# Kernel tuning notes

Measured on AMD Instinct MI355X. Metric: run time of the kernel, lower is better.

The kernel has to match this reference:

```python
import jax, jax.numpy as jnp
import numpy as np

B, S, T, E, H = 64, 128, 128, 512, 1024


def setup_inputs() -> dict:
    key = jax.random.key(0)
    ks = jax.random.split(key, 12)

    def lin(k, shape, fan_in):
        return jax.random.normal(k, shape, jnp.float32) / np.float32(np.sqrt(fan_in))

    return {
        "trg_embed": jax.random.normal(ks[0], (B, T, E), jnp.float32),
        "encoder_hidden": jax.random.normal(ks[1], (B, S, 2 * H), jnp.float32),
        "encoder_final": jax.random.normal(ks[2], (B, 2 * H), jnp.float32),
        "src_mask": jnp.ones((B, S), dtype=bool),
        # BahdanauAttention params (all bias=False)
        "key_W": lin(ks[3], (H, 2 * H), 2 * H),      # proj_key = enc_hidden @ key_W.T
        "query_W": lin(ks[4], (H, H), H),
        "energy_w": lin(ks[5], (H,), H),             # energy_layer Linear(H, 1)
        # GRU (single layer) params, PyTorch layout [3H, in] with gate order r,z,n
        "W_ih": lin(ks[6], (3 * H, E + 2 * H), E + 2 * H),
        "W_hh": lin(ks[7], (3 * H, H), H),
        "b_ih": jnp.zeros((3 * H,), jnp.float32),
        "b_hh": jnp.zeros((3 * H,), jnp.float32),
        # bridge Linear(2H, H, bias=True)
        "bridge_W": lin(ks[8], (H, 2 * H), 2 * H),
        "bridge_b": jnp.zeros((H,), jnp.float32),
        # pre_output_layer Linear(H + 2H + E, H, bias=False)
        "preout_W": lin(ks[9], (H, 3 * H + E), 3 * H + E),
    }


def reference(trg_embed, encoder_hidden, encoder_final, src_mask,
              key_W, query_W, energy_w, W_ih, W_hh, b_ih, b_hh,
              bridge_W, bridge_b, preout_W):
    # Precompute attention keys once: [B, S, H]
    proj_key = jnp.einsum('bsd,hd->bsh', encoder_hidden, key_W)
    # init_hidden: tanh(bridge(encoder_final)) -> [B, H]
    h0 = jnp.tanh(encoder_final @ bridge_W.T + bridge_b)
    neg = jnp.asarray(-1e9, trg_embed.dtype)

    def step(h, prev_embed):  # h: [B,H], prev_embed: [B,E]
        # Bahdanau attention
        q = h @ query_W.T                                            # [B,H]
        scores = jnp.einsum('bsh,h->bs',
                            jnp.tanh(q[:, None, :] + proj_key), energy_w)  # [B,S]
        scores = jnp.where(src_mask, scores, neg)
        alphas = jax.nn.softmax(scores, axis=-1)
        context = jnp.einsum('bs,bsd->bd', alphas, encoder_hidden)   # [B,2H]
        # GRU cell (PyTorch gate math)
        x = jnp.concatenate([prev_embed, context], axis=-1)          # [B,E+2H]
        gi = x @ W_ih.T + b_ih
        gh = h @ W_hh.T + b_hh
        ir, iz, in_ = jnp.split(gi, 3, axis=-1)
        hr, hz, hn = jnp.split(gh, 3, axis=-1)
        r = jax.nn.sigmoid(ir + hr)
        z = jax.nn.sigmoid(iz + hz)
        n = jnp.tanh(in_ + r * hn)
        h_new = (1.0 - z) * n + z * h                                # [B,H]
        # pre-output projection (dropout is identity in eval / p=0)
        pre = jnp.concatenate([prev_embed, h_new, context], axis=-1) @ preout_W.T
        return h_new, (h_new, pre)

    h_final, (states, pre_outputs) = jax.lax.scan(step, h0,
                                                  jnp.swapaxes(trg_embed, 0, 1))
    decoder_states = jnp.swapaxes(states, 0, 1)        # [B,T,H]
    pre_output_vectors = jnp.swapaxes(pre_outputs, 0, 1)  # [B,T,H]
    return decoder_states, h_final, pre_output_vectors
```

## Files before the change

### kernel.cpp

```cpp
#include <hip/hip_runtime.h>
#include <hip/hip_bf16.h>

#define DI __device__ __forceinline__
typedef __attribute__((ext_vector_type(8))) short bf16x8;
typedef __attribute__((ext_vector_type(4))) float f32x4;
typedef unsigned short u16;

namespace {

constexpr int B_ = 64, S_ = 128, T_ = 128, E_ = 512, H_ = 1024;

DI float bf2f(u16 v){ unsigned u = ((unsigned)v)<<16; float f; __builtin_memcpy(&f,&u,4); return f; }
DI u16 f2bf(float x){ unsigned u; __builtin_memcpy(&u,&x,4); u += 0x7fffu + ((u>>16)&1u); return (u16)(u>>16); }

template<int SRC>
DI void stage(const void* A, int lda, int row, int k, u16* dst){
  if constexpr(SRC==0){
    *(bf16x8*)dst = *(const bf16x8*)((const u16*)A + (size_t)row*lda + k);
  } else {
    const float* a = (const float*)A + (size_t)row*lda + k;
    float4 v0 = *(const float4*)a;
    float4 v1 = *(const float4*)(a+4);
    bf16x8 r;
    r[0]=(short)f2bf(v0.x); r[1]=(short)f2bf(v0.y); r[2]=(short)f2bf(v0.z); r[3]=(short)f2bf(v0.w);
    r[4]=(short)f2bf(v1.x); r[5]=(short)f2bf(v1.y); r[6]=(short)f2bf(v1.z); r[7]=(short)f2bf(v1.w);
    *(bf16x8*)dst = r;
  }
}

template<int ASRC, int BSRC, bool OBF16>
DI void gemm_tile(const void* __restrict__ A, int lda,
                  const void* __restrict__ Bw, int ldb,
                  void* __restrict__ out, int ldout,
                  int m0, int n0, int k0, int Kc,
                  u16* As, u16* Bs)
{
  constexpr int LS = 72;
  int tid = threadIdx.x;
  int w = tid>>6, l = tid&63;
  f32x4 acc0{0,0,0,0}, acc1{0,0,0,0}, acc2{0,0,0,0}, acc3{0,0,0,0};
  int sr = tid>>2, sk = (tid&3)*8;
  u16* asw = &As[sr*LS+sk];
  u16* bsw = &Bs[sr*LS+sk];
  int arow = (l&15)*LS + (l>>4)*8;
  for(int kk=0; kk<Kc; kk+=64){
    stage<ASRC>(A, lda, m0+sr, k0+kk+sk,    asw);
    stage<ASRC>(A, lda, m0+sr, k0+kk+32+sk, asw+32);
    stage<BSRC>(Bw, ldb, n0+sr, k0+kk+sk,    bsw);
    stage<BSRC>(Bw, ldb, n0+sr, k0+kk+32+sk, bsw+32);
    __syncthreads();
    #pragma unroll
    for(int c=0;c<2;c++){
      bf16x8 bf = *(const bf16x8*)&Bs[w*16*LS + arow + c*32];
      bf16x8 a0 = *(const bf16x8*)&As[0*16*LS + arow + c*32];
      bf16x8 a1 = *(const bf16x8*)&As[1*16*LS + arow + c*32];
      bf16x8 a2 = *(const bf16x8*)&As[2*16*LS + arow + c*32];
      bf16x8 a3 = *(const bf16x8*)&As[3*16*LS + arow + c*32];
      acc0 = __builtin_amdgcn_mfma_f32_16x16x32_bf16(a0, bf, acc0, 0,0,0);
      acc1 = __builtin_amdgcn_mfma_f32_16x16x32_bf16(a1, bf, acc1, 0,0,0);
      acc2 = __builtin_amdgcn_mfma_f32_16x16x32_bf16(a2, bf, acc2, 0,0,0);
      acc3 = __builtin_amdgcn_mfma_f32_16x16x32_bf16(a3, bf, acc3, 0,0,0);
    }
    __syncthreads();
  }
  int col = n0 + w*16 + (l&15);
  int rbase = m0 + (l>>4)*4;
  f32x4 av[4] = {acc0, acc1, acc2, acc3};
  #pragma unroll
  for(int mb=0; mb<4; mb++){
    #pragma unroll
    for(int r=0; r<4; r++){
      int row = rbase + mb*16 + r;
      float v = av[mb][r];
      if(OBF16) ((u16*)out)[(size_t)row*ldout + col] = f2bf(v);
      else      ((float*)out)[(size_t)row*ldout + col] = v;
    }
  }
}

template<int ASRC, int BSRC, bool OBF16>
__global__ __launch_bounds__(256) void k_gemm(
  const void* __restrict__ A, int lda, const void* __restrict__ Bw, int ldb,
  void* __restrict__ out, int N, int n_tiles, int splits, int Kc, int spStride)
{
  __shared__ u16 As[64*72], Bs[64*72];
  int bid = blockIdx.x;
  int sp = bid % splits;
  int nt = (bid/splits) % n_tiles;
  int mt = bid/(splits*n_tiles);
  void* o = out;
  if(!OBF16) o = (void*)((float*)out + (size_t)sp*spStride);
  gemm_tile<ASRC,BSRC,OBF16>(A, lda, Bw, ldb, o, N, mt*64, nt*64, sp*Kc, Kc, As, Bs);
}

__global__ __launch_bounds__(256) void k_step1(
  const u16* __restrict__ h_bf, const u16* __restrict__ qW,
  const u16* __restrict__ hhW, const u16* __restrict__ poWh,
  float* __restrict__ Pq, float* __restrict__ Pgh, float* __restrict__ Ppre, int t)
{
  __shared__ u16 As[64*72], Bs[64*72];
  int bid = blockIdx.x;
  if(bid < 64){
    int sp = bid & 3, nt = bid >> 2;
    gemm_tile<0,0,false>(h_bf, H_, qW, H_, Pq + sp*(64*1024), 1024, 0, nt*64, sp*256, 256, As, Bs);
  } else if(bid < 256){
    int b2 = bid-64; int sp = b2 & 3, nt = b2 >> 2;
    gemm_tile<0,0,false>(h_bf, H_, hhW, H_, Pgh + sp*(64*3072), 3072, 0, nt*64, sp*256, 256, As, Bs);
  } else {
    if(t == 0) return;
    int b2 = bid-256; int sp = b2 & 3, nt = b2 >> 2;
    gemm_tile<0,0,false>(h_bf, H_, poWh, H_, Ppre + sp*(64*1024), 1024, 0, nt*64, sp*256, 256, As, Bs);
  }
}

DI void presum4(int b, int tid, int tm1,
                const float* __restrict__ Ppre, const u16* __restrict__ poe,
                const float* __restrict__ pctx, float* __restrict__ out_pre)
{
  int o = tid*4;
  float a0=0,a1=0,a2=0,a3=0;
  #pragma unroll
  for(int sp=0; sp<4; sp++){
    const float* q = &Ppre[(size_t)(sp*64 + b)*1024 + o];
    a0+=q[0]; a1+=q[1]; a2+=q[2]; a3+=q[3];
  }
  const u16* pe = &poe[((size_t)b*T_ + tm1)*1024 + o];
  a0 += bf2f(pe[0]); a1 += bf2f(pe[1]); a2 += bf2f(pe[2]); a3 += bf2f(pe[3]);
  const float* pc = &pctx[(size_t)b*1024 + o];
  a0 += pc[0]; a1 += pc[1]; a2 += pc[2]; a3 += pc[3];
  float* d = &out_pre[((size_t)b*T_ + tm1)*1024 + o];
  d[0]=a0; d[1]=a1; d[2]=a2; d[3]=a3;
}

__global__ __launch_bounds__(256) void k_step2(
  const float* __restrict__ Pq, const u16* __restrict__ pk_bf,
  const float* __restrict__ ew, float* __restrict__ scores,
  const float* __restrict__ Ppre, const u16* __restrict__ poe,
  const float* __restrict__ pctx, float* __restrict__ out_pre, int t)
{
  int bid = blockIdx.x, tid = threadIdx.x;
  if(bid >= 512){
    if(t > 0) presum4(bid-512, tid, t-1, Ppre, poe, pctx, out_pre);
    return;
  }
  __shared__ float qs[1024], ws[1024];
  int b = bid >> 3, sc = bid & 7;
  {
    int hdx = tid*4;
    float4 a = *(const float4*)&Pq[(size_t)b*1024 + hdx];
    #pragma unroll
    for(int sp=1; sp<4; sp++){
      float4 q = *(const float4*)&Pq[(size_t)(sp*64+b)*1024 + hdx];
      a.x+=q.x; a.y+=q.y; a.z+=q.z; a.w+=q.w;
    }
    *(float4*)&qs[hdx] = a;
    *(float4*)&ws[hdx] = *(const float4*)&ew[hdx];
  }
  __syncthreads();
  int w = tid>>6, l = tid&63;
  #pragma unroll
  for(int si=0; si<4; si++){
    int s = sc*16 + w*4 + si;
    const u16* pk = &pk_bf[((size_t)b*S_ + s)*1024 + l];
    float acc = 0.f;
    #pragma unroll
    for(int j=0;j<16;j++){
      float x = qs[l + j*64] + bf2f(pk[j*64]);
      acc += tanhf(x) * ws[l + j*64];
    }
    #pragma unroll
    for(int off=32; off; off>>=1) acc += __shfl_xor(acc, off, 64);
    if(l==0) scores[b*S_ + s] = acc;
  }
}

__global__ __launch_bounds__(256) void k_step3(
  const float* __restrict__ scores, const u16* __restrict__ EHgi,
  const u16* __restrict__ EHpo, const float* __restrict__ Pgh,
  const u16* __restrict__ gie, const float* __restrict__ bih,
  const float* __restrict__ bhh, float* __restrict__ h,
  u16* __restrict__ h_bf, float* __restrict__ pctx,
  float* __restrict__ out_states, int t)
{
  __shared__ float al[128];
  __shared__ float red[4][128];
  int b = blockIdx.x >> 3, jc = blockIdx.x & 7;
  int tid = threadIdx.x;
  if(tid < 128) al[tid] = scores[b*S_ + tid];
  __syncthreads();
  float m = -1e30f;
  #pragma unroll 1
  for(int s=0;s<128;s++) m = fmaxf(m, al[s]);
  float e = (tid < 128) ? expf(al[tid]-m) : 0.f;
  __syncthreads();
  if(tid < 128) al[tid] = e;
  __syncthreads();
  float sum = 0.f;
  #pragma unroll 1
  for(int s=0;s<128;s++) sum += al[s];
  float rs = 1.f/sum;

  int grp = tid>>6, lt = tid&63;
  const u16* src; int rstride;
  if(grp < 3){ src = EHgi + (size_t)b*S_*3072 + grp*1024 + jc*128 + lt*2; rstride = 3072; }
  else       { src = EHpo + (size_t)b*S_*1024 +            jc*128 + lt*2; rstride = 1024; }
  float a0=0.f, a1=0.f;
  #pragma unroll 8
  for(int s=0;s<128;s++){
    unsigned pv = *(const unsigned*)(src + (size_t)s*rstride);
    float als = al[s];
    a0 += als * bf2f((u16)(pv & 0xffffu));
    a1 += als * bf2f((u16)(pv >> 16));
  }
  red[grp][lt*2]   = a0;
  red[grp][lt*2+1] = a1;
  __syncthreads();

  if(tid < 128){
    int jj = jc*128 + tid;
    float gir = red[0][tid]*rs, giz = red[1][tid]*rs, gin = red[2][tid]*rs;
    float pox = red[3][tid]*rs;
    float ghr=0.f, ghz=0.f, ghn=0.f;
    #pragma unroll
    for(int sp=0;sp<4;sp++){
      const float* pg = &Pgh[(size_t)(sp*64+b)*3072 + jj];
      ghr += pg[0]; ghz += pg[1024]; ghn += pg[2048];
    }
    size_t eo = ((size_t)b*T_ + t)*3072 + jj;
    gir += bf2f(gie[eo])      + bih[jj];
    giz += bf2f(gie[eo+1024]) + bih[jj+1024];
    gin += bf2f(gie[eo+2048]) + bih[jj+2048];
    ghr += bhh[jj]; ghz += bhh[jj+1024]; ghn += bhh[jj+2048];
    float r = 1.f/(1.f+expf(-(gir+ghr)));
    float z = 1.f/(1.f+expf(-(giz+ghz)));
    float n = tanhf(gin + r*ghn);
    float hold = h[b*1024+jj];
    float hnew = (1.f - z)*n + z*hold;
    h[b*1024+jj] = hnew;
    h_bf[b*1024+jj] = f2bf(hnew);
    out_states[((size_t)b*T_ + t)*1024 + jj] = hnew;
    pctx[b*1024+jj] = pox;
  }
}

__global__ __launch_bounds__(256) void k_h0fin(
  const float* __restrict__ P, const float* __restrict__ brb,
  float* __restrict__ h, u16* __restrict__ h_bf)
{
  int gid = blockIdx.x*256 + threadIdx.x;
  int b = gid >> 10, o = gid & 1023;
  float a = brb[o];
  #pragma unroll
  for(int sp=0; sp<8; sp++) a += P[(size_t)(sp*64+b)*1024 + o];
  float hv = tanhf(a);
  h[gid] = hv;
  h_bf[gid] = f2bf(hv);
}

__global__ __launch_bounds__(256) void k_presum(
  const float* __restrict__ Ppre, const u16* __restrict__ poe,
  const float* __restrict__ pctx, float* __restrict__ out_pre, int tm1)
{
  presum4(blockIdx.x, threadIdx.x, tm1, Ppre, poe, pctx, out_pre);
}

__global__ __launch_bounds__(256) void k_cvt(const float* __restrict__ s, u16* __restrict__ d, int n){
  int i = (blockIdx.x*256 + threadIdx.x)*4;
  if(i >= n) return;
  float4 v = *(const float4*)&s[i];
  d[i]=f2bf(v.x); d[i+1]=f2bf(v.y); d[i+2]=f2bf(v.z); d[i+3]=f2bf(v.w);
}

__global__ __launch_bounds__(256) void k_cvtcols(const float* __restrict__ s, u16* __restrict__ d,
                                                 int src_ld, int c0){
  int idx = (blockIdx.x*256 + threadIdx.x)*4;
  int row = idx >> 10, col = idx & 1023;
  float4 v = *(const float4*)&s[(size_t)row*src_ld + c0 + col];
  d[idx]=f2bf(v.x); d[idx+1]=f2bf(v.y); d[idx+2]=f2bf(v.z); d[idx+3]=f2bf(v.w);
}

}

extern "C" void kernel_launch(void* const* d_in, const int* in_sizes, int n_in,
                              void* d_out, int out_size, void* d_ws, size_t ws_size,
                              hipStream_t stream)
{
  const float* trg  = (const float*)d_in[0];
  const float* eh   = (const float*)d_in[1];
  const float* ef   = (const float*)d_in[2];
  const float* keyW = (const float*)d_in[4];
  const float* qW   = (const float*)d_in[5];
  const float* ew   = (const float*)d_in[6];
  const float* Wih  = (const float*)d_in[7];
  const float* Whh  = (const float*)d_in[8];
  const float* bih  = (const float*)d_in[9];
  const float* bhh  = (const float*)d_in[10];
  const float* brW  = (const float*)d_in[11];
  const float* brb  = (const float*)d_in[12];
  const float* poW  = (const float*)d_in[13];

  float* out = (float*)d_out;
  float* out_states = out;
  float* out_hfin   = out + (size_t)B_*T_*H_;
  float* out_pre    = out_hfin + (size_t)B_*H_;

  char* p = (char*)d_ws;
  auto carve = [&](size_t bytes)->char*{ char* r=p; p += (bytes+255)&~(size_t)255; return r; };
  u16* pk_bf   = (u16*)carve((size_t)B_*S_*H_*2);
  u16* gie_bf  = (u16*)carve((size_t)B_*T_*3*H_*2);
  u16* poe_bf  = (u16*)carve((size_t)B_*T_*H_*2);
  u16* EHgi    = (u16*)carve((size_t)B_*S_*3*H_*2);
  u16* EHpo    = (u16*)carve((size_t)B_*S_*H_*2);
  u16* qW_bf   = (u16*)carve((size_t)H_*H_*2);
  u16* Whh_bf  = (u16*)carve((size_t)3*H_*H_*2);
  u16* poWh_bf = (u16*)carve((size_t)H_*H_*2);
  float* Pq    = (float*)carve((size_t)4*64*1024*4);
  float* Pgh   = (float*)carve((size_t)4*64*3072*4);
  float* Ppre  = (float*)carve((size_t)8*64*1024*4);
  float* pctx  = (float*)carve((size_t)B_*H_*4);
  float* h     = (float*)carve((size_t)B_*H_*4);
  u16*  h_bf   = (u16*)carve((size_t)B_*H_*2);
  float* scores= (float*)carve((size_t)B_*S_*4);
  (void)ws_size; (void)in_sizes; (void)n_in; (void)out_size;

  k_cvt<<<1024,256,0,stream>>>(qW,  qW_bf,  H_*H_);
  k_cvt<<<3072,256,0,stream>>>(Whh, Whh_bf, 3*H_*H_);
  k_cvtcols<<<1024,256,0,stream>>>(poW, poWh_bf, 3*H_+E_, E_);

  k_gemm<1,1,true><<<2048,256,0,stream>>>(eh, 2048, keyW, 2048, pk_bf, 1024, 16, 1, 2048, 0);
  k_gemm<1,1,true><<<6144,256,0,stream>>>(trg, 512, Wih, 2560, gie_bf, 3072, 48, 1, 512, 0);
  k_gemm<1,1,true><<<2048,256,0,stream>>>(trg, 512, poW, 3584, poe_bf, 1024, 16, 1, 512, 0);
  k_gemm<1,1,true><<<6144,256,0,stream>>>(eh, 2048, Wih + E_, 2560, EHgi, 3072, 48, 1, 2048, 0);
  k_gemm<1,1,true><<<2048,256,0,stream>>>(eh, 2048, poW + E_ + H_, 3584, EHpo, 1024, 16, 1, 2048, 0);
  k_gemm<1,1,false><<<128,256,0,stream>>>(ef, 2048, brW, 2048, Ppre, 1024, 16, 8, 256, 64*1024);
  k_h0fin<<<256,256,0,stream>>>(Ppre, brb, h, h_bf);

  for(int t=0; t<T_; ++t){
    k_step1<<<320,256,0,stream>>>(h_bf, qW_bf, Whh_bf, poWh_bf, Pq, Pgh, Ppre, t);
    k_step2<<<576,256,0,stream>>>(Pq, pk_bf, ew, scores, Ppre, poe_bf, pctx, out_pre, t);
    k_step3<<<512,256,0,stream>>>(scores, EHgi, EHpo, Pgh, gie_bf, bih, bhh,
                                  h, h_bf, pctx, out_states, t);
  }

  k_gemm<0,0,false><<<64,256,0,stream>>>(h_bf, H_, poWh_bf, H_, Ppre, 1024, 16, 4, 256, 64*1024);
  k_presum<<<64,256,0,stream>>>(Ppre, poe_bf, pctx, out_pre, T_-1);
  hipMemcpyAsync(out_hfin, h, (size_t)B_*H_*4, hipMemcpyDeviceToDevice, stream);
}
```

Measured before the change: 8.321 ms.

## Fuse per-step recurrence kernels into one persistent kernel with grid barriers

Replaces the 384 per-timestep kernel launches (three kernels per step) with a single persistent kernel of 512 blocks. Stages are separated by atomic-counter grid barriers, and the final pre-output projection and h_final copy are folded into an extra iteration. The W_hh GEMM now uses an 8-way K split so its 384 blocks fill the grid alongside the other GEMMs. Launch overhead and inter-kernel gaps are removed. In exchange, correctness depends on all 512 blocks being co-resident (two blocks per CU are required), and the spin barriers add their own cost.

```diff
diff --git a/kernel.cpp b/kernel.cpp
--- a/kernel.cpp
+++ b/kernel.cpp
@@ -9,6 +9,7 @@
 namespace {
 
 constexpr int B_ = 64, S_ = 128, T_ = 128, E_ = 512, H_ = 1024;
+constexpr unsigned NBLK = 512;
 
 DI float bf2f(u16 v){ unsigned u = ((unsigned)v)<<16; float f; __builtin_memcpy(&f,&u,4); return f; }
 DI u16 f2bf(float x){ unsigned u; __builtin_memcpy(&u,&x,4); u += 0x7fffu + ((u>>16)&1u); return (u16)(u>>16); }
@@ -93,26 +94,6 @@
   gemm_tile<ASRC,BSRC,OBF16>(A, lda, Bw, ldb, o, N, mt*64, nt*64, sp*Kc, Kc, As, Bs);
 }
 
-__global__ __launch_bounds__(256) void k_step1(
-  const u16* __restrict__ h_bf, const u16* __restrict__ qW,
-  const u16* __restrict__ hhW, const u16* __restrict__ poWh,
-  float* __restrict__ Pq, float* __restrict__ Pgh, float* __restrict__ Ppre, int t)
-{
-  __shared__ u16 As[64*72], Bs[64*72];
-  int bid = blockIdx.x;
-  if(bid < 64){
-    int sp = bid & 3, nt = bid >> 2;
-    gemm_tile<0,0,false>(h_bf, H_, qW, H_, Pq + sp*(64*1024), 1024, 0, nt*64, sp*256, 256, As, Bs);
-  } else if(bid < 256){
-    int b2 = bid-64; int sp = b2 & 3, nt = b2 >> 2;
-    gemm_tile<0,0,false>(h_bf, H_, hhW, H_, Pgh + sp*(64*3072), 3072, 0, nt*64, sp*256, 256, As, Bs);
-  } else {
-    if(t == 0) return;
-    int b2 = bid-256; int sp = b2 & 3, nt = b2 >> 2;
-    gemm_tile<0,0,false>(h_bf, H_, poWh, H_, Ppre + sp*(64*1024), 1024, 0, nt*64, sp*256, 256, As, Bs);
-  }
-}
-
 DI void presum4(int b, int tid, int tm1,
                 const float* __restrict__ Ppre, const u16* __restrict__ poe,
                 const float* __restrict__ pctx, float* __restrict__ out_pre)
@@ -132,114 +113,148 @@
   d[0]=a0; d[1]=a1; d[2]=a2; d[3]=a3;
 }
 
-__global__ __launch_bounds__(256) void k_step2(
-  const float* __restrict__ Pq, const u16* __restrict__ pk_bf,
-  const float* __restrict__ ew, float* __restrict__ scores,
-  const float* __restrict__ Ppre, const u16* __restrict__ poe,
-  const float* __restrict__ pctx, float* __restrict__ out_pre, int t)
-{
+DI void grid_barrier(unsigned* cnt){
+  __syncthreads();
+  if(threadIdx.x==0){
+    __builtin_amdgcn_fence(__ATOMIC_RELEASE, "agent");
+    unsigned old = __hip_atomic_fetch_add(cnt, 1u, __ATOMIC_RELAXED, __HIP_MEMORY_SCOPE_AGENT);
+    unsigned target = (old/NBLK + 1u)*NBLK;
+    while(__hip_atomic_load(cnt, __ATOMIC_RELAXED, __HIP_MEMORY_SCOPE_AGENT) < target)
+      __builtin_amdgcn_s_sleep(1);
+    __builtin_amdgcn_fence(__ATOMIC_ACQUIRE, "agent");
+  }
+  __syncthreads();
+}
+
+struct LoopArgs {
+  const u16 *pk, *gie, *poe, *EHgi, *EHpo, *qW, *Whh, *poWh;
+  const float *ew, *bih, *bhh;
+  float *Pq, *Pgh, *Ppre, *pctx, *h, *scores, *out_states, *out_pre, *out_hfin;
+  u16 *h_bf;
+  unsigned *cnt;
+};
+
+__global__ __launch_bounds__(256, 2) void k_loop(LoopArgs a)
+{
+  __shared__ __align__(16) char lds_raw[18432];
+  u16* As = (u16*)lds_raw;
+  u16* Bs = As + 64*72;
   int bid = blockIdx.x, tid = threadIdx.x;
-  if(bid >= 512){
-    if(t > 0) presum4(bid-512, tid, t-1, Ppre, poe, pctx, out_pre);
-    return;
-  }
-  __shared__ float qs[1024], ws[1024];
-  int b = bid >> 3, sc = bid & 7;
-  {
-    int hdx = tid*4;
-    float4 a = *(const float4*)&Pq[(size_t)b*1024 + hdx];
-    #pragma unroll
-    for(int sp=1; sp<4; sp++){
-      float4 q = *(const float4*)&Pq[(size_t)(sp*64+b)*1024 + hdx];
-      a.x+=q.x; a.y+=q.y; a.z+=q.z; a.w+=q.w;
-    }
-    *(float4*)&qs[hdx] = a;
-    *(float4*)&ws[hdx] = *(const float4*)&ew[hdx];
-  }
-  __syncthreads();
-  int w = tid>>6, l = tid&63;
-  #pragma unroll
-  for(int si=0; si<4; si++){
-    int s = sc*16 + w*4 + si;
-    const u16* pk = &pk_bf[((size_t)b*S_ + s)*1024 + l];
-    float acc = 0.f;
-    #pragma unroll
-    for(int j=0;j<16;j++){
-      float x = qs[l + j*64] + bf2f(pk[j*64]);
-      acc += tanhf(x) * ws[l + j*64];
-    }
-    #pragma unroll
-    for(int off=32; off; off>>=1) acc += __shfl_xor(acc, off, 64);
-    if(l==0) scores[b*S_ + s] = acc;
-  }
-}
-
-__global__ __launch_bounds__(256) void k_step3(
-  const float* __restrict__ scores, const u16* __restrict__ EHgi,
-  const u16* __restrict__ EHpo, const float* __restrict__ Pgh,
-  const u16* __restrict__ gie, const float* __restrict__ bih,
-  const float* __restrict__ bhh, float* __restrict__ h,
-  u16* __restrict__ h_bf, float* __restrict__ pctx,
-  float* __restrict__ out_states, int t)
-{
-  __shared__ float al[128];
-  __shared__ float red[4][128];
-  int b = blockIdx.x >> 3, jc = blockIdx.x & 7;
-  int tid = threadIdx.x;
-  if(tid < 128) al[tid] = scores[b*S_ + tid];
-  __syncthreads();
-  float m = -1e30f;
-  #pragma unroll 1
-  for(int s=0;s<128;s++) m = fmaxf(m, al[s]);
-  float e = (tid < 128) ? expf(al[tid]-m) : 0.f;
-  __syncthreads();
-  if(tid < 128) al[tid] = e;
-  __syncthreads();
-  float sum = 0.f;
-  #pragma unroll 1
-  for(int s=0;s<128;s++) sum += al[s];
-  float rs = 1.f/sum;
-
-  int grp = tid>>6, lt = tid&63;
-  const u16* src; int rstride;
-  if(grp < 3){ src = EHgi + (size_t)b*S_*3072 + grp*1024 + jc*128 + lt*2; rstride = 3072; }
-  else       { src = EHpo + (size_t)b*S_*1024 +            jc*128 + lt*2; rstride = 1024; }
-  float a0=0.f, a1=0.f;
-  #pragma unroll 8
-  for(int s=0;s<128;s++){
-    unsigned pv = *(const unsigned*)(src + (size_t)s*rstride);
-    float als = al[s];
-    a0 += als * bf2f((u16)(pv & 0xffffu));
-    a1 += als * bf2f((u16)(pv >> 16));
-  }
-  red[grp][lt*2]   = a0;
-  red[grp][lt*2+1] = a1;
-  __syncthreads();
-
-  if(tid < 128){
-    int jj = jc*128 + tid;
-    float gir = red[0][tid]*rs, giz = red[1][tid]*rs, gin = red[2][tid]*rs;
-    float pox = red[3][tid]*rs;
-    float ghr=0.f, ghz=0.f, ghn=0.f;
-    #pragma unroll
-    for(int sp=0;sp<4;sp++){
-      const float* pg = &Pgh[(size_t)(sp*64+b)*3072 + jj];
-      ghr += pg[0]; ghz += pg[1024]; ghn += pg[2048];
-    }
-    size_t eo = ((size_t)b*T_ + t)*3072 + jj;
-    gir += bf2f(gie[eo])      + bih[jj];
-    giz += bf2f(gie[eo+1024]) + bih[jj+1024];
-    gin += bf2f(gie[eo+2048]) + bih[jj+2048];
-    ghr += bhh[jj]; ghz += bhh[jj+1024]; ghn += bhh[jj+2048];
-    float r = 1.f/(1.f+expf(-(gir+ghr)));
-    float z = 1.f/(1.f+expf(-(giz+ghz)));
-    float n = tanhf(gin + r*ghn);
-    float hold = h[b*1024+jj];
-    float hnew = (1.f - z)*n + z*hold;
-    h[b*1024+jj] = hnew;
-    h_bf[b*1024+jj] = f2bf(hnew);
-    out_states[((size_t)b*T_ + t)*1024 + jj] = hnew;
-    pctx[b*1024+jj] = pox;
+
+  for(int t=0; t<=T_; ++t){
+    if(bid < 64){
+      if(t < T_){ int sp=bid&3, nt=bid>>2;
+        gemm_tile<0,0,false>(a.h_bf,H_,a.qW,H_, a.Pq+sp*(64*1024),1024, 0,nt*64, sp*256,256, As,Bs); }
+    } else if(bid < 448){
+      if(t < T_){ int b2=bid-64, sp=b2&7, nt=b2>>3;
+        gemm_tile<0,0,false>(a.h_bf,H_,a.Whh,H_, a.Pgh+sp*(64*3072),3072, 0,nt*64, sp*128,128, As,Bs); }
+    } else {
+      if(t > 0){ int b2=bid-448, sp=b2&3, nt=b2>>2;
+        gemm_tile<0,0,false>(a.h_bf,H_,a.poWh,H_, a.Ppre+sp*(64*1024),1024, 0,nt*64, sp*256,256, As,Bs); }
+    }
+    grid_barrier(a.cnt);
+
+    {
+      int b = bid>>3, sc = bid&7;
+      if(t < T_){
+        float* qs = (float*)lds_raw;
+        float* ws = qs + 1024;
+        int hdx = tid*4;
+        float4 av = *(const float4*)&a.Pq[(size_t)b*1024 + hdx];
+        #pragma unroll
+        for(int sp=1; sp<4; sp++){
+          float4 q = *(const float4*)&a.Pq[(size_t)(sp*64+b)*1024 + hdx];
+          av.x+=q.x; av.y+=q.y; av.z+=q.z; av.w+=q.w;
+        }
+        *(float4*)&qs[hdx] = av;
+        *(float4*)&ws[hdx] = *(const float4*)&a.ew[hdx];
+        __syncthreads();
+        int w = tid>>6, l = tid&63;
+        #pragma unroll
+        for(int si=0; si<4; si++){
+          int s = sc*16 + w*4 + si;
+          const u16* pkp = &a.pk[((size_t)b*S_ + s)*1024 + l];
+          float acc = 0.f;
+          #pragma unroll
+          for(int j=0;j<16;j++){
+            float x = qs[l + j*64] + bf2f(pkp[j*64]);
+            acc += tanhf(x) * ws[l + j*64];
+          }
+          #pragma unroll
+          for(int off=32; off; off>>=1) acc += __shfl_xor(acc, off, 64);
+          if(l==0) a.scores[b*S_ + s] = acc;
+        }
+      }
+      if(sc==7 && t>0) presum4(b, tid, t-1, a.Ppre, a.poe, a.pctx, a.out_pre);
+      if(sc==0 && t==T_){
+        int o = tid*4;
+        *(float4*)&a.out_hfin[(size_t)b*1024+o] = *(const float4*)&a.h[(size_t)b*1024+o];
+      }
+    }
+    if(t == T_) break;
+    grid_barrier(a.cnt);
+
+    {
+      float* al  = (float*)lds_raw;
+      float* red = al + 128;
+      int b = bid>>3, jc = bid&7;
+      if(tid < 128) al[tid] = a.scores[b*S_ + tid];
+      __syncthreads();
+      float m = -1e30f;
+      #pragma unroll 1
+      for(int s=0;s<128;s++) m = fmaxf(m, al[s]);
+      float e = (tid < 128) ? expf(al[tid]-m) : 0.f;
+      __syncthreads();
+      if(tid < 128) al[tid] = e;
+      __syncthreads();
+      float sum = 0.f;
+      #pragma unroll 1
+      for(int s=0;s<128;s++) sum += al[s];
+      float rs = 1.f/sum;
+
+      int grp = tid>>6, lt = tid&63;
+      const u16* src; int rstride;
+      if(grp < 3){ src = a.EHgi + (size_t)b*S_*3072 + grp*1024 + jc*128 + lt*2; rstride = 3072; }
+      else       { src = a.EHpo + (size_t)b*S_*1024 +            jc*128 + lt*2; rstride = 1024; }
+      float a0=0.f, a1=0.f;
+      #pragma unroll 8
+      for(int s=0;s<128;s++){
+        unsigned pv = *(const unsigned*)(src + (size_t)s*rstride);
+        float als = al[s];
+        a0 += als * bf2f((u16)(pv & 0xffffu));
+        a1 += als * bf2f((u16)(pv >> 16));
+      }
+      red[grp*128 + lt*2]   = a0;
+      red[grp*128 + lt*2+1] = a1;
+      __syncthreads();
+
+      if(tid < 128){
+        int jj = jc*128 + tid;
+        float gir = red[0*128+tid]*rs, giz = red[1*128+tid]*rs, gin = red[2*128+tid]*rs;
+        float pox = red[3*128+tid]*rs;
+        float ghr=0.f, ghz=0.f, ghn=0.f;
+        #pragma unroll
+        for(int sp=0;sp<8;sp++){
+          const float* pg = &a.Pgh[(size_t)(sp*64+b)*3072 + jj];
+          ghr += pg[0]; ghz += pg[1024]; ghn += pg[2048];
+        }
+        size_t eo = ((size_t)b*T_ + t)*3072 + jj;
+        gir += bf2f(a.gie[eo])      + a.bih[jj];
+        giz += bf2f(a.gie[eo+1024]) + a.bih[jj+1024];
+        gin += bf2f(a.gie[eo+2048]) + a.bih[jj+2048];
+        ghr += a.bhh[jj]; ghz += a.bhh[jj+1024]; ghn += a.bhh[jj+2048];
+        float r = 1.f/(1.f+expf(-(gir+ghr)));
+        float z = 1.f/(1.f+expf(-(giz+ghz)));
+        float n = tanhf(gin + r*ghn);
+        float hold = a.h[b*1024+jj];
+        float hnew = (1.f - z)*n + z*hold;
+        a.h[b*1024+jj] = hnew;
+        a.h_bf[b*1024+jj] = f2bf(hnew);
+        a.out_states[((size_t)b*T_ + t)*1024 + jj] = hnew;
+        a.pctx[b*1024+jj] = pox;
+      }
+    }
+    grid_barrier(a.cnt);
   }
 }
 
@@ -257,12 +272,7 @@
   h_bf[gid] = f2bf(hv);
 }
 
-__global__ __launch_bounds__(256) void k_presum(
-  const float* __restrict__ Ppre, const u16* __restrict__ poe,
-  const float* __restrict__ pctx, float* __restrict__ out_pre, int tm1)
-{
-  presum4(blockIdx.x, threadIdx.x, tm1, Ppre, poe, pctx, out_pre);
-}
+__global__ void k_zero(unsigned* c){ if(threadIdx.x==0) *c = 0u; }
 
 __global__ __launch_bounds__(256) void k_cvt(const float* __restrict__ s, u16* __restrict__ d, int n){
   int i = (blockIdx.x*256 + threadIdx.x)*4;
@@ -315,12 +325,13 @@
   u16* Whh_bf  = (u16*)carve((size_t)3*H_*H_*2);
   u16* poWh_bf = (u16*)carve((size_t)H_*H_*2);
   float* Pq    = (float*)carve((size_t)4*64*1024*4);
-  float* Pgh   = (float*)carve((size_t)4*64*3072*4);
+  float* Pgh   = (float*)carve((size_t)8*64*3072*4);
   float* Ppre  = (float*)carve((size_t)8*64*1024*4);
   float* pctx  = (float*)carve((size_t)B_*H_*4);
   float* h     = (float*)carve((size_t)B_*H_*4);
   u16*  h_bf   = (u16*)carve((size_t)B_*H_*2);
   float* scores= (float*)carve((size_t)B_*S_*4);
+  unsigned* cnt= (unsigned*)carve(256);
   (void)ws_size; (void)in_sizes; (void)n_in; (void)out_size;
 
   k_cvt<<<1024,256,0,stream>>>(qW,  qW_bf,  H_*H_);
@@ -334,15 +345,14 @@
   k_gemm<1,1,true><<<2048,256,0,stream>>>(eh, 2048, poW + E_ + H_, 3584, EHpo, 1024, 16, 1, 2048, 0);
   k_gemm<1,1,false><<<128,256,0,stream>>>(ef, 2048, brW, 2048, Ppre, 1024, 16, 8, 256, 64*1024);
   k_h0fin<<<256,256,0,stream>>>(Ppre, brb, h, h_bf);
-
-  for(int t=0; t<T_; ++t){
-    k_step1<<<320,256,0,stream>>>(h_bf, qW_bf, Whh_bf, poWh_bf, Pq, Pgh, Ppre, t);
-    k_step2<<<576,256,0,stream>>>(Pq, pk_bf, ew, scores, Ppre, poe_bf, pctx, out_pre, t);
-    k_step3<<<512,256,0,stream>>>(scores, EHgi, EHpo, Pgh, gie_bf, bih, bhh,
-                                  h, h_bf, pctx, out_states, t);
-  }
-
-  k_gemm<0,0,false><<<64,256,0,stream>>>(h_bf, H_, poWh_bf, H_, Ppre, 1024, 16, 4, 256, 64*1024);
-  k_presum<<<64,256,0,stream>>>(Ppre, poe_bf, pctx, out_pre, T_-1);
-  hipMemcpyAsync(out_hfin, h, (size_t)B_*H_*4, hipMemcpyDeviceToDevice, stream);
-}
+  k_zero<<<1,64,0,stream>>>(cnt);
+
+  LoopArgs la;
+  la.pk = pk_bf; la.gie = gie_bf; la.poe = poe_bf; la.EHgi = EHgi; la.EHpo = EHpo;
+  la.qW = qW_bf; la.Whh = Whh_bf; la.poWh = poWh_bf;
+  la.ew = ew; la.bih = bih; la.bhh = bhh;
+  la.Pq = Pq; la.Pgh = Pgh; la.Ppre = Ppre; la.pctx = pctx; la.h = h;
+  la.scores = scores; la.out_states = out_states; la.out_pre = out_pre;
+  la.out_hfin = out_hfin; la.h_bf = h_bf; la.cnt = cnt;
+  k_loop<<<NBLK,256,0,stream>>>(la);
+}
```

Result: slower. 27.97 ms (+236.1%).
